# Kernel optimization log

Hardware: AMD Instinct MI355X
Metric: run time of the kernel (lower is better)

Reference implementation:

```python
import jax, jax.numpy as jnp
import numpy as np

EPS = 1e-5

def bn_eval(x, p):
    # p: [4, C] = gamma, beta, running_mean, running_var; channel-last broadcast
    g, b, m, v = p[0], p[1], p[2], p[3]
    return (x - m) * (g / jnp.sqrt(v + EPS)) + b

def _bn_params(k, c):
    k1, k2, k3, k4 = jax.random.split(k, 4)
    gamma = jax.random.uniform(k1, (c,)) + 0.5
    beta = jax.random.normal(k2, (c,)) * 0.1
    mean = jax.random.normal(k3, (c,)) * 0.1
    var = jax.random.uniform(k4, (c,)) + 0.5
    return jnp.stack([gamma, beta, mean, var])

def _lin(k, fan_in, fan_out):
    bound = 1.0 / np.sqrt(fan_in)
    kw, kb = jax.random.split(k)
    w = jax.random.uniform(kw, (fan_in, fan_out), minval=-bound, maxval=bound)
    b = jax.random.uniform(kb, (fan_out,), minval=-bound, maxval=bound)
    return w, b

def setup_inputs() -> dict:
    key = jax.random.key(0)
    B, N, S, C, G = 2, 4096, 16, 256, 8
    ks = jax.random.split(key, 20)
    feats = jax.random.normal(ks[0], (B, N, C), dtype=jnp.float32)
    coords = jax.random.normal(ks[1], (B, N, 3), dtype=jnp.float32)
    index = jax.random.randint(ks[2], (B, N, S), 0, N, dtype=jnp.int32)
    wq, bq = _lin(ks[3], C, C); bnq = _bn_params(ks[4], C)
    wk, bk = _lin(ks[5], C, C); bnk = _bn_params(ks[6], C)
    wv, bv = _lin(ks[7], C, C)
    pm_w1, pm_b1 = _lin(ks[8], 3, C); pm_bn = _bn_params(ks[9], C)
    pm_w2, pm_b2 = _lin(ks[10], C, C)
    pb_w1, pb_b1 = _lin(ks[11], 3, C); pb_bn = _bn_params(ks[12], C)
    pb_w2, pb_b2 = _lin(ks[13], C, C)
    we_w1, we_b1 = _lin(ks[14], C, G); we_bn = _bn_params(ks[15], G)
    we_w2, we_b2 = _lin(ks[16], G, G)
    return dict(feats=feats, coords=coords, index=index,
                wq=wq, bq=bq, bnq=bnq, wk=wk, bk=bk, bnk=bnk, wv=wv, bv=bv,
                pm_w1=pm_w1, pm_b1=pm_b1, pm_bn=pm_bn, pm_w2=pm_w2, pm_b2=pm_b2,
                pb_w1=pb_w1, pb_b1=pb_b1, pb_bn=pb_bn, pb_w2=pb_w2, pb_b2=pb_b2,
                we_w1=we_w1, we_b1=we_b1, we_bn=we_bn, we_w2=we_w2, we_b2=we_b2)

def reference(feats, coords, index,
              wq, bq, bnq, wk, bk, bnk, wv, bv,
              pm_w1, pm_b1, pm_bn, pm_w2, pm_b2,
              pb_w1, pb_b1, pb_bn, pb_w2, pb_b2,
              we_w1, we_b1, we_bn, we_w2, we_b2):
    B, N, C = feats.shape
    S = index.shape[2]
    G = we_w1.shape[1]
    q = jax.nn.relu(bn_eval(feats @ wq + bq, bnq))                       # [B,N,C]
    k = jax.nn.relu(bn_eval(feats @ wk + bk, bnk))                       # [B,N,C]
    v = feats @ wv + bv                                                   # [B,N,C]
    idx = index.reshape(B, N * S)
    key_g = jnp.take_along_axis(k, idx[:, :, None], axis=1).reshape(B, N, S, C)
    val_g = jnp.take_along_axis(v, idx[:, :, None], axis=1).reshape(B, N, S, C)
    crd_g = jnp.take_along_axis(coords, idx[:, :, None], axis=1).reshape(B, N, S, 3)
    relation_qk = key_g - q[:, :, None, :]                                # [B,N,S,C]
    pos = coords[:, :, None, :] - crd_g                                   # [B,N,S,3]
    pem = jax.nn.relu(bn_eval(pos @ pm_w1 + pm_b1, pm_bn)) @ pm_w2 + pm_b2
    relation_qk = relation_qk * pem
    peb = jax.nn.relu(bn_eval(pos @ pb_w1 + pb_b1, pb_bn)) @ pb_w2 + pb_b2
    relation_qk = relation_qk + peb
    val_g = val_g + peb
    w = jax.nn.relu(bn_eval(relation_qk @ we_w1 + we_b1, we_bn)) @ we_w2 + we_b2  # [B,N,S,G]
    w = jax.nn.softmax(w, axis=2)                                         # softmax over neighbors
    val_g = val_g.reshape(B, N, S, G, C // G)
    out = jnp.einsum('bnsgi,bnsg->bngi', val_g, w).reshape(B, N, C)
    return out
```

## Files before the change

kernel.cpp:

```cpp
#include <hip/hip_runtime.h>
#include <hip/hip_bf16.h>


typedef __attribute__((ext_vector_type(8))) short bf16x8_t;
typedef __attribute__((ext_vector_type(4))) float f32x4_t;

#define BN_EPS 1e-5f
#define WSYNC() asm volatile("s_waitcnt lgkmcnt(0)" ::: "memory")

__device__ __forceinline__ float blo(unsigned int v) {
    union { unsigned int u; float f; } x; x.u = v << 16; return x.f;
}
__device__ __forceinline__ float bhi(unsigned int v) {
    union { unsigned int u; float f; } x; x.u = v & 0xffff0000u; return x.f;
}
__device__ __forceinline__ unsigned int fbits(float f) {
    union { float f; unsigned int u; } x; x.f = f; return x.u;
}
__device__ __forceinline__ unsigned short f2b(float f) {
    unsigned int u = fbits(f);
    return (unsigned short)((u + 0x7fffu + ((u >> 16) & 1u)) >> 16);
}
__device__ __forceinline__ float b2f(unsigned short h) {
    union { unsigned int u; float f; } x; x.u = ((unsigned int)h) << 16; return x.f;
}
__device__ __forceinline__ unsigned int f2bpk(float a, float b) {
    union { __hip_bfloat162 h; unsigned int u; } x;
    x.h = __float22bfloat162_rn(make_float2(a, b));
    return x.u;
}
__device__ __forceinline__ unsigned int relpair(unsigned int kb, unsigned int qb,
                                                unsigned int pm_, unsigned int pb_) {
    float r0 = (blo(kb) - blo(qb)) * blo(pm_) + blo(pb_);
    float r1 = (bhi(kb) - bhi(qb)) * bhi(pm_) + bhi(pb_);
    return f2bpk(r0, r1);
}

__global__ __launch_bounds__(256) void k_prep(
    const float* __restrict__ wq, const float* __restrict__ wk,
    const float* __restrict__ wv, const float* __restrict__ pm2,
    const float* __restrict__ pb2,
    const float* __restrict__ pm_w1, const float* __restrict__ pm_b1,
    const float* __restrict__ pm_bn,
    const float* __restrict__ pb_w1, const float* __restrict__ pb_b1,
    const float* __restrict__ pb_bn,
    const float* __restrict__ we_w1,
    unsigned short* __restrict__ wsT, unsigned short* __restrict__ w1F,
    unsigned short* __restrict__ we1TF)
{
    const int bid = blockIdx.x, t = threadIdx.x;
    if (bid < 160) {
        __shared__ unsigned short T[32][72];
        const int mat = bid >> 5;
        const int kk  = (bid >> 2) & 7;
        const int ntq = bid & 3;
        const float* s = (mat == 0) ? wq : (mat == 1) ? wk : (mat == 2) ? wv
                         : (mat == 3) ? pm2 : pb2;
        {
            int c = t & 63, r0 = t >> 6;
            for (int i = 0; i < 8; ++i) {
                int r = r0 + i * 4;
                T[r][c] = f2b(s[(kk * 32 + r) * 256 + ntq * 64 + c]);
            }
        }
        __syncthreads();
        {
            int seg = t >> 6, lane = t & 63;
            int col = seg * 16 + (lane & 15);
            int kr  = (lane >> 4) * 8;
            unsigned int v[8];
            #pragma unroll
            for (int j = 0; j < 8; ++j) v[j] = T[kr + j][col];
            uint4 o;
            o.x = v[0] | (v[1] << 16);
            o.y = v[2] | (v[3] << 16);
            o.z = v[4] | (v[5] << 16);
            o.w = v[6] | (v[7] << 16);
            *(uint4*)(wsT + mat * 65536 + (ntq * 4 + seg) * 4096 + kk * 512 + lane * 8) = o;
        }
    } else if (bid == 160) {
        int c = t;
        int nt = c >> 4, l15 = c & 15;
        float sm = pm_bn[c] / sqrtf(pm_bn[768 + c] + BN_EPS);
        float sb = pb_bn[c] / sqrtf(pb_bn[768 + c] + BN_EPS);
        float W[2][4];
        W[0][0] = pm_w1[c] * sm; W[0][1] = pm_w1[256 + c] * sm;
        W[0][2] = pm_w1[512 + c] * sm;
        W[0][3] = (pm_b1[c] - pm_bn[512 + c]) * sm + pm_bn[256 + c];
        W[1][0] = pb_w1[c] * sb; W[1][1] = pb_w1[256 + c] * sb;
        W[1][2] = pb_w1[512 + c] * sb;
        W[1][3] = (pb_b1[c] - pb_bn[512 + c]) * sb + pb_bn[256 + c];
        for (int pass = 0; pass < 2; ++pass) {
            unsigned short xh = f2b(W[pass][0]), xl = f2b(W[pass][0] - b2f(xh));
            unsigned short yh = f2b(W[pass][1]), yl = f2b(W[pass][1] - b2f(yh));
            unsigned short zh = f2b(W[pass][2]), zl = f2b(W[pass][2] - b2f(zh));
            unsigned short bh = f2b(W[pass][3]), bl = f2b(W[pass][3] - b2f(bh));
            unsigned short sl[16] = { xh, xh, xl, yh, yh, yl, zh, zh, zl,
                                      bh, bl, 0, 0, 0, 0, 0 };
            for (int q = 0; q < 4; ++q)
                for (int j = 0; j < 8; ++j)
                    w1F[((pass * 16 + nt) * 64 + q * 16 + l15) * 8 + j] =
                        (q < 2) ? sl[q * 8 + j] : (unsigned short)0;
        }
    } else {
        for (int j = 0; j < 8; ++j) {
            int e = t * 8 + j;
            int g = e >> 8, c = e & 255;
            we1TF[g * 256 + c] = f2b(we_w1[c * 8 + g]);
        }
    }
}

__global__ __launch_bounds__(256) void k_qkv(
    const float* __restrict__ feats,
    const unsigned short* __restrict__ wT,
    const float* __restrict__ bq, const float* __restrict__ bnq,
    const float* __restrict__ bk, const float* __restrict__ bnk,
    const float* __restrict__ bv,
    unsigned short* __restrict__ qkv)
{
    __shared__ unsigned short A[32][264];
    const int t    = threadIdx.x;
    const int widx = blockIdx.x >> 8;
    const int mb   = blockIdx.x & 255;

    for (int i = 0; i < 8; ++i) {
        int row = 4 * i + (t >> 6), col = (t & 63) * 4;
        float4 f = *(const float4*)(feats + (mb * 32 + row) * 256 + col);
        *(uint2*)&A[row][col] = make_uint2(f2bpk(f.x, f.y), f2bpk(f.z, f.w));
    }
    __syncthreads();

    const int lane = t & 63, w = t >> 6;
    const int ln15 = lane & 15, quad = lane >> 4;
    const int mt = w & 1, nh = w >> 1;

    bf16x8_t afr[8];
    #pragma unroll
    for (int kk = 0; kk < 8; ++kk)
        afr[kk] = *(const bf16x8_t*)&A[mt * 16 + ln15][kk * 32 + quad * 8];

    const unsigned short* W = wT + widx * 65536;
    const float* bias = (widx == 0) ? bq : (widx == 1) ? bk : bv;
    const float* bn   = (widx == 0) ? bnq : (widx == 1) ? bnk : nullptr;
    unsigned short* dst = qkv + (size_t)widx * 8192 * 256;

    f32x4_t acc[8];
    for (int j = 0; j < 8; ++j) acc[j] = (f32x4_t){0.f, 0.f, 0.f, 0.f};

    #pragma unroll
    for (int kk = 0; kk < 8; ++kk) {
        #pragma unroll
        for (int j = 0; j < 8; ++j) {
            int nt = nh * 8 + j;
            bf16x8_t bfr = *(const bf16x8_t*)(W + ((nt * 8 + kk) * 64 + lane) * 8);
            acc[j] = __builtin_amdgcn_mfma_f32_16x16x32_bf16(afr[kk], bfr, acc[j], 0, 0, 0);
        }
    }

    float bb[8], sc[8], mu[8], be[8];
    #pragma unroll
    for (int j = 0; j < 8; ++j) {
        int c = (nh * 8 + j) * 16 + ln15;
        bb[j] = bias[c];
        if (bn) {
            sc[j] = bn[c] / sqrtf(bn[768 + c] + BN_EPS);
            be[j] = bn[256 + c];
            mu[j] = bn[512 + c];
        }
    }
    __syncthreads();
    #pragma unroll
    for (int j = 0; j < 8; ++j) {
        int c = (nh * 8 + j) * 16 + ln15;
        float y[4];
        for (int r = 0; r < 4; ++r) {
            y[r] = acc[j][r] + bb[j];
            if (bn) y[r] = fmaxf((y[r] - mu[j]) * sc[j] + be[j], 0.f);
        }
        for (int r = 0; r < 4; r += 2) {
            unsigned int pk = f2bpk(y[r], y[r + 1]);
            A[mt * 16 + quad * 4 + r][c]     = (unsigned short)pk;
            A[mt * 16 + quad * 4 + r + 1][c] = (unsigned short)(pk >> 16);
        }
    }
    __syncthreads();
    {
        int row = t >> 3, cc = (t & 7) * 32;
        #pragma unroll
        for (int j = 0; j < 4; ++j) {
            uint4 v = *(const uint4*)&A[row][cc + 8 * j];
            *(uint4*)(dst + (mb * 32 + row) * 256 + cc + 8 * j) = v;
        }
    }
}

__global__ __launch_bounds__(512, 4) void k_main(
    const float* __restrict__ coords,
    const int*   __restrict__ index,
    const unsigned short* __restrict__ qm,
    const unsigned short* __restrict__ km,
    const unsigned short* __restrict__ vm,
    const unsigned short* __restrict__ pmw2F,
    const unsigned short* __restrict__ pbw2F,
    const unsigned short* __restrict__ w1F,
    const unsigned short* __restrict__ we1TF,
    const float* __restrict__ pm_b2, const float* __restrict__ pb_b2,
    const float* __restrict__ we_b1, const float* __restrict__ we_bn,
    const float* __restrict__ we_w2, const float* __restrict__ we_b2,
    float* __restrict__ out)
{
    __shared__ unsigned short bufR[64][264];
    __shared__ unsigned short bufP[64][264];
    __shared__ unsigned short posX[64][32];
    __shared__ float usP[2][64][8];
    __shared__ float us_[64][8];
    __shared__ int   rowg_[64];
    __shared__ float we2s[8][8];
    __shared__ float web2[8], swe8[8], dwe8[8];

    const int t   = threadIdx.x;
    const int P0  = blockIdx.x * 4;
    const int bb_ = P0 >> 12;
    const int w = t >> 6, lane = t & 63;
    const int ln15 = lane & 15, quad = lane >> 4;
    const int p   = w >> 1, sub = w & 1;
    const int R0  = p * 16;
    const int Pg  = P0 + p;

    const int rg = (bb_ << 12) + index[Pg * 16 + ln15];
    uint4 kpre[4];
    #pragma unroll
    for (int kk = 0; kk < 4; ++kk)
        kpre[kk] = *(const uint4*)(km + rg * 256 + (sub * 4 + kk) * 32 + quad * 8);

    if (t < 64) {
        int m  = t;
        int Pr = P0 + (m >> 4);
        int rs = (bb_ << 12) + index[Pr * 16 + (m & 15)];
        rowg_[m] = rs;
        float x = coords[Pr * 3 + 0] - coords[rs * 3 + 0];
        float y = coords[Pr * 3 + 1] - coords[rs * 3 + 1];
        float z = coords[Pr * 3 + 2] - coords[rs * 3 + 2];
        unsigned short xh = f2b(x), xl = f2b(x - b2f(xh));
        unsigned short yh = f2b(y), yl = f2b(y - b2f(yh));
        unsigned short zh = f2b(z), zl = f2b(z - b2f(zh));
        const unsigned short one = 0x3f80;
        posX[m][0] = xh; posX[m][1] = xl; posX[m][2] = xh;
        posX[m][3] = yh; posX[m][4] = yl; posX[m][5] = yh;
        posX[m][6] = zh; posX[m][7] = zl; posX[m][8] = zh;
        posX[m][9] = one; posX[m][10] = one;
        #pragma unroll
        for (int j2 = 11; j2 < 32; ++j2) posX[m][j2] = 0;
        we2s[m >> 3][m & 7] = we_w2[m];
    }
    if (t < 8) {
        float s = we_bn[t] / sqrtf(we_bn[24 + t] + BN_EPS);
        swe8[t] = s;
        dwe8[t] = (we_b1[t] - we_bn[16 + t]) * s + we_bn[8 + t];
        web2[t] = we_b2[t];
    }
    __syncthreads();

    bf16x8_t afrP[4];
    #pragma unroll
    for (int mt = 0; mt < 4; ++mt)
        afrP[mt] = *(const bf16x8_t*)&posX[mt * 16 + ln15][quad * 8];

    {
        f32x4_t hb[2][4];
        for (int ntl = 0; ntl < 2; ++ntl)
            for (int mt = 0; mt < 4; ++mt) hb[ntl][mt] = (f32x4_t){0.f, 0.f, 0.f, 0.f};
        #pragma unroll
        for (int ntl = 0; ntl < 2; ++ntl) {
            int nt = w * 2 + ntl;
            bf16x8_t wfr = *(const bf16x8_t*)(w1F + ((16 + nt) * 64 + lane) * 8);
            #pragma unroll
            for (int mt = 0; mt < 4; ++mt)
                hb[ntl][mt] = __builtin_amdgcn_mfma_f32_16x16x32_bf16(wfr, afrP[mt], hb[ntl][mt], 0, 0, 0);
        }
        #pragma unroll
        for (int ntl = 0; ntl < 2; ++ntl) {
            int cb = w * 32 + ntl * 16 + quad * 4;
            #pragma unroll
            for (int mt = 0; mt < 4; ++mt) {
                unsigned int pk0 = f2bpk(fmaxf(hb[ntl][mt][0], 0.f), fmaxf(hb[ntl][mt][1], 0.f));
                unsigned int pk1 = f2bpk(fmaxf(hb[ntl][mt][2], 0.f), fmaxf(hb[ntl][mt][3], 0.f));
                *(uint2*)&bufR[mt * 16 + ln15][cb] = make_uint2(pk0, pk1);
            }
        }
    }
    __syncthreads();

    f32x4_t accM[2][4];
    for (int ntl = 0; ntl < 2; ++ntl)
        for (int mt = 0; mt < 4; ++mt) accM[ntl][mt] = (f32x4_t){0.f, 0.f, 0.f, 0.f};
    #pragma unroll
    for (int ntl = 0; ntl < 2; ++ntl) {
        int nt = w * 2 + ntl;
        bf16x8_t wfr = *(const bf16x8_t*)(w1F + (nt * 64 + lane) * 8);
        #pragma unroll
        for (int mt = 0; mt < 4; ++mt)
            accM[ntl][mt] = __builtin_amdgcn_mfma_f32_16x16x32_bf16(wfr, afrP[mt], accM[ntl][mt], 0, 0, 0);
    }
    f32x4_t acc[2][4];
    {
        f32x4_t b0 = *(const f32x4_t*)(pb_b2 + (w * 2    ) * 16 + quad * 4);
        f32x4_t b1 = *(const f32x4_t*)(pb_b2 + (w * 2 + 1) * 16 + quad * 4);
        for (int mt = 0; mt < 4; ++mt) { acc[0][mt] = b0; acc[1][mt] = b1; }
    }
    #pragma unroll
    for (int kk = 0; kk < 8; ++kk) {
        bf16x8_t afr[4];
        #pragma unroll
        for (int mt = 0; mt < 4; ++mt)
            afr[mt] = *(const bf16x8_t*)&bufR[mt * 16 + ln15][kk * 32 + quad * 8];
        #pragma unroll
        for (int ntl = 0; ntl < 2; ++ntl) {
            int nt = w * 2 + ntl;
            bf16x8_t wfr = *(const bf16x8_t*)(pbw2F + ((nt * 8 + kk) * 64 + lane) * 8);
            #pragma unroll
            for (int mt = 0; mt < 4; ++mt)
                acc[ntl][mt] = __builtin_amdgcn_mfma_f32_16x16x32_bf16(wfr, afr[mt], acc[ntl][mt], 0, 0, 0);
        }
    }
    #pragma unroll
    for (int ntl = 0; ntl < 2; ++ntl) {
        int cb = w * 32 + ntl * 16 + quad * 4;
        #pragma unroll
        for (int mt = 0; mt < 4; ++mt) {
            unsigned int pk0 = f2bpk(acc[ntl][mt][0], acc[ntl][mt][1]);
            unsigned int pk1 = f2bpk(acc[ntl][mt][2], acc[ntl][mt][3]);
            *(uint2*)&bufP[mt * 16 + ln15][cb] = make_uint2(pk0, pk1);
        }
    }
    __syncthreads();

    #pragma unroll
    for (int ntl = 0; ntl < 2; ++ntl) {
        int cb = w * 32 + ntl * 16 + quad * 4;
        #pragma unroll
        for (int mt = 0; mt < 4; ++mt) {
            unsigned int pk0 = f2bpk(fmaxf(accM[ntl][mt][0], 0.f), fmaxf(accM[ntl][mt][1], 0.f));
            unsigned int pk1 = f2bpk(fmaxf(accM[ntl][mt][2], 0.f), fmaxf(accM[ntl][mt][3], 0.f));
            *(uint2*)&bufR[mt * 16 + ln15][cb] = make_uint2(pk0, pk1);
        }
    }
    __syncthreads();

    uint4 qpre[4];
    #pragma unroll
    for (int kk = 0; kk < 4; ++kk)
        qpre[kk] = *(const uint4*)(qm + Pg * 256 + (sub * 4 + kk) * 32 + quad * 8);
    {
        f32x4_t b0 = *(const f32x4_t*)(pm_b2 + (w * 2    ) * 16 + quad * 4);
        f32x4_t b1 = *(const f32x4_t*)(pm_b2 + (w * 2 + 1) * 16 + quad * 4);
        for (int mt = 0; mt < 4; ++mt) { acc[0][mt] = b0; acc[1][mt] = b1; }
    }
    #pragma unroll
    for (int kk = 0; kk < 8; ++kk) {
        bf16x8_t afr[4];
        #pragma unroll
        for (int mt = 0; mt < 4; ++mt)
            afr[mt] = *(const bf16x8_t*)&bufR[mt * 16 + ln15][kk * 32 + quad * 8];
        #pragma unroll
        for (int ntl = 0; ntl < 2; ++ntl) {
            int nt = w * 2 + ntl;
            bf16x8_t wfr = *(const bf16x8_t*)(pmw2F + ((nt * 8 + kk) * 64 + lane) * 8);
            #pragma unroll
            for (int mt = 0; mt < 4; ++mt)
                acc[ntl][mt] = __builtin_amdgcn_mfma_f32_16x16x32_bf16(wfr, afr[mt], acc[ntl][mt], 0, 0, 0);
        }
    }
    __syncthreads();

    #pragma unroll
    for (int ntl = 0; ntl < 2; ++ntl) {
        int cb = w * 32 + ntl * 16 + quad * 4;
        #pragma unroll
        for (int mt = 0; mt < 4; ++mt) {
            unsigned int pk0 = f2bpk(acc[ntl][mt][0], acc[ntl][mt][1]);
            unsigned int pk1 = f2bpk(acc[ntl][mt][2], acc[ntl][mt][3]);
            *(uint2*)&bufR[mt * 16 + ln15][cb] = make_uint2(pk0, pk1);
        }
    }
    __syncthreads();

    {
        const bf16x8_t bz = {0, 0, 0, 0, 0, 0, 0, 0};
        f32x4_t lacc = {0.f, 0.f, 0.f, 0.f};
        #pragma unroll
        for (int kk = 0; kk < 4; ++kk) {
            int cb8 = (sub * 4 + kk) * 32 + quad * 8;
            uint4 pm4 = *(const uint4*)&bufR[R0 + ln15][cb8];
            uint4 pb4 = *(const uint4*)&bufP[R0 + ln15][cb8];
            uint4 q4  = qpre[kk];
            union { uint4 u; bf16x8_t v; } rr;
            rr.u.x = relpair(kpre[kk].x, q4.x, pm4.x, pb4.x);
            rr.u.y = relpair(kpre[kk].y, q4.y, pm4.y, pb4.y);
            rr.u.z = relpair(kpre[kk].z, q4.z, pm4.z, pb4.z);
            rr.u.w = relpair(kpre[kk].w, q4.w, pm4.w, pb4.w);
            bf16x8_t wfr = bz;
            if (ln15 < 8) wfr = *(const bf16x8_t*)(we1TF + ln15 * 256 + cb8);
            lacc = __builtin_amdgcn_mfma_f32_16x16x32_bf16(wfr, rr.v, lacc, 0, 0, 0);
        }
        if (quad < 2)
            *(f32x4_t*)&usP[sub][R0 + ln15][quad * 4] = lacc;
    }
    __syncthreads();

    if (sub == 0 && lane < 16) {
        int s = lane;
        float uv[8], l[8];
        #pragma unroll
        for (int g = 0; g < 8; ++g) {
            float x = usP[0][R0 + s][g] + usP[1][R0 + s][g];
            uv[g] = fmaxf(x * swe8[g] + dwe8[g], 0.f);
        }
        #pragma unroll
        for (int g = 0; g < 8; ++g) {
            float x = web2[g];
            for (int gp = 0; gp < 8; ++gp) x += uv[gp] * we2s[gp][g];
            l[g] = x;
        }
        #pragma unroll
        for (int g = 0; g < 8; ++g) us_[R0 + s][g] = l[g];
    }
    WSYNC();

    if (sub == 0 && lane < 8) {
        int g = lane;
        float mx = -1e30f;
        for (int s = 0; s < 16; ++s) mx = fmaxf(mx, us_[R0 + s][g]);
        float e[16], sum = 0.f;
        for (int s = 0; s < 16; ++s) { e[s] = __expf(us_[R0 + s][g] - mx); sum += e[s]; }
        float inv = 1.f / sum;
        for (int s = 0; s < 16; ++s) us_[R0 + s][g] = e[s] * inv;
    }
    __syncthreads();

    {
        int idx2 = sub * 64 + lane;
        int c5 = idx2 * 2, g = c5 >> 5;
        float a0 = 0.f, a1 = 0.f;
        #pragma unroll
        for (int s = 0; s < 16; ++s) {
            int rv = rowg_[R0 + s];
            float wv_ = us_[R0 + s][g];
            unsigned int v2 = *(const unsigned int*)(vm + rv * 256 + c5);
            unsigned int p2 = *(const unsigned int*)&bufP[R0 + s][c5];
            a0 += wv_ * (blo(v2) + blo(p2));
            a1 += wv_ * (bhi(v2) + bhi(p2));
        }
        *(float2*)(out + (size_t)Pg * 256 + c5) = make_float2(a0, a1);
    }
}

extern "C" void kernel_launch(void* const* d_in, const int* in_sizes, int n_in,
                              void* d_out, int out_size, void* d_ws, size_t ws_size,
                              hipStream_t stream)
{
    const float* feats  = (const float*)d_in[0];
    const float* coords = (const float*)d_in[1];
    const int*   index  = (const int*)d_in[2];
    const float* wq     = (const float*)d_in[3];
    const float* bq     = (const float*)d_in[4];
    const float* bnq    = (const float*)d_in[5];
    const float* wk     = (const float*)d_in[6];
    const float* bk     = (const float*)d_in[7];
    const float* bnk    = (const float*)d_in[8];
    const float* wv     = (const float*)d_in[9];
    const float* bv     = (const float*)d_in[10];
    const float* pm_w1  = (const float*)d_in[11];
    const float* pm_b1  = (const float*)d_in[12];
    const float* pm_bn  = (const float*)d_in[13];
    const float* pm_w2  = (const float*)d_in[14];
    const float* pm_b2  = (const float*)d_in[15];
    const float* pb_w1  = (const float*)d_in[16];
    const float* pb_b1  = (const float*)d_in[17];
    const float* pb_bn  = (const float*)d_in[18];
    const float* pb_w2  = (const float*)d_in[19];
    const float* pb_b2  = (const float*)d_in[20];
    const float* we_w1  = (const float*)d_in[21];
    const float* we_b1  = (const float*)d_in[22];
    const float* we_bn  = (const float*)d_in[23];
    const float* we_w2  = (const float*)d_in[24];
    const float* we_b2  = (const float*)d_in[25];

    unsigned short* qkv   = (unsigned short*)d_ws;
    unsigned short* wsT   = qkv + (size_t)3 * 8192 * 256;
    unsigned short* we1TF = wsT + 5 * 65536;
    unsigned short* w1F   = we1TF + 2048;

    const size_t need = (size_t)13275136;
    if (ws_size < need) {
        hipMemsetAsync(d_out, 0, (size_t)out_size * 4, stream);
        return;
    }

    k_prep<<<162,  256, 0, stream>>>(wq, wk, wv, pm_w2, pb_w2,
                                     pm_w1, pm_b1, pm_bn,
                                     pb_w1, pb_b1, pb_bn,
                                     we_w1, wsT, w1F, we1TF);
    k_qkv <<<768,  256, 0, stream>>>(feats, wsT, bq, bnq, bk, bnk, bv, qkv);
    k_main<<<2048, 512, 0, stream>>>(coords, index,
                                     qkv,
                                     qkv + (size_t)8192 * 256,
                                     qkv + (size_t)2 * 8192 * 256,
                                     wsT + 3 * 65536,
                                     wsT + 4 * 65536,
                                     w1F, we1TF,
                                     pm_b2, pb_b2,
                                     we_b1, we_bn, we_w2, we_b2,
                                     (float*)d_out);
}
```

Measured before the change: 191.3 us.

## Fold BN into scale/shift, drop LDS staging, split relation reduction per wave

Precomputes per-channel BN scale/shift for q/k/v in the prep kernel. k_qkv swaps the MFMA operand order so each lane writes four consecutive channels straight to global, removing the LDS staging and two barriers. In k_main each wave now covers the full 256-channel reduction for its own point, so the cross-subwave partial sums and block-level syncs go away. Value gathers are prefetched into registers using shuffled row indices. The cost is higher register pressure from 8 k/q prefetches plus 16 value loads per lane, which may hurt occupancy.

```diff
diff --git a/kernel.cpp b/kernel.cpp
--- a/kernel.cpp
+++ b/kernel.cpp
@@ -45,8 +45,11 @@
     const float* __restrict__ pb_w1, const float* __restrict__ pb_b1,
     const float* __restrict__ pb_bn,
     const float* __restrict__ we_w1,
+    const float* __restrict__ bq, const float* __restrict__ bnq,
+    const float* __restrict__ bk, const float* __restrict__ bnk,
+    const float* __restrict__ bv,
     unsigned short* __restrict__ wsT, unsigned short* __restrict__ w1F,
-    unsigned short* __restrict__ we1TF)
+    unsigned short* __restrict__ we1TF, float* __restrict__ SS)
 {
     const int bid = blockIdx.x, t = threadIdx.x;
     if (bid < 160) {
@@ -108,15 +111,22 @@
             int g = e >> 8, c = e & 255;
             we1TF[g * 256 + c] = f2b(we_w1[c * 8 + g]);
         }
+        int c = t;
+        float sq = bnq[c] / sqrtf(bnq[768 + c] + BN_EPS);
+        SS[c]        = sq;
+        SS[256 + c]  = (bq[c] - bnq[512 + c]) * sq + bnq[256 + c];
+        float sk = bnk[c] / sqrtf(bnk[768 + c] + BN_EPS);
+        SS[512 + c]  = sk;
+        SS[768 + c]  = (bk[c] - bnk[512 + c]) * sk + bnk[256 + c];
+        SS[1024 + c] = 1.0f;
+        SS[1280 + c] = bv[c];
     }
 }
 
 __global__ __launch_bounds__(256) void k_qkv(
     const float* __restrict__ feats,
     const unsigned short* __restrict__ wT,
-    const float* __restrict__ bq, const float* __restrict__ bnq,
-    const float* __restrict__ bk, const float* __restrict__ bnk,
-    const float* __restrict__ bv,
+    const float* __restrict__ SS,
     unsigned short* __restrict__ qkv)
 {
     __shared__ unsigned short A[32][264];
@@ -141,8 +151,6 @@
         afr[kk] = *(const bf16x8_t*)&A[mt * 16 + ln15][kk * 32 + quad * 8];
 
     const unsigned short* W = wT + widx * 65536;
-    const float* bias = (widx == 0) ? bq : (widx == 1) ? bk : bv;
-    const float* bn   = (widx == 0) ? bnq : (widx == 1) ? bnk : nullptr;
     unsigned short* dst = qkv + (size_t)widx * 8192 * 256;
 
     f32x4_t acc[8];
@@ -153,45 +161,28 @@
         #pragma unroll
         for (int j = 0; j < 8; ++j) {
             int nt = nh * 8 + j;
-            bf16x8_t bfr = *(const bf16x8_t*)(W + ((nt * 8 + kk) * 64 + lane) * 8);
-            acc[j] = __builtin_amdgcn_mfma_f32_16x16x32_bf16(afr[kk], bfr, acc[j], 0, 0, 0);
-        }
-    }
-
-    float bb[8], sc[8], mu[8], be[8];
+            bf16x8_t wfr = *(const bf16x8_t*)(W + ((nt * 8 + kk) * 64 + lane) * 8);
+            acc[j] = __builtin_amdgcn_mfma_f32_16x16x32_bf16(wfr, afr[kk], acc[j], 0, 0, 0);
+        }
+    }
+
+    const float* S = SS + widx * 512;
+    const int row = mb * 32 + mt * 16 + ln15;
     #pragma unroll
     for (int j = 0; j < 8; ++j) {
-        int c = (nh * 8 + j) * 16 + ln15;
-        bb[j] = bias[c];
-        if (bn) {
-            sc[j] = bn[c] / sqrtf(bn[768 + c] + BN_EPS);
-            be[j] = bn[256 + c];
-            mu[j] = bn[512 + c];
-        }
-    }
-    __syncthreads();
-    #pragma unroll
-    for (int j = 0; j < 8; ++j) {
-        int c = (nh * 8 + j) * 16 + ln15;
-        float y[4];
-        for (int r = 0; r < 4; ++r) {
-            y[r] = acc[j][r] + bb[j];
-            if (bn) y[r] = fmaxf((y[r] - mu[j]) * sc[j] + be[j], 0.f);
-        }
-        for (int r = 0; r < 4; r += 2) {
-            unsigned int pk = f2bpk(y[r], y[r + 1]);
-            A[mt * 16 + quad * 4 + r][c]     = (unsigned short)pk;
-            A[mt * 16 + quad * 4 + r + 1][c] = (unsigned short)(pk >> 16);
-        }
-    }
-    __syncthreads();
-    {
-        int row = t >> 3, cc = (t & 7) * 32;
-        #pragma unroll
-        for (int j = 0; j < 4; ++j) {
-            uint4 v = *(const uint4*)&A[row][cc + 8 * j];
-            *(uint4*)(dst + (mb * 32 + row) * 256 + cc + 8 * j) = v;
-        }
+        int n0 = (nh * 8 + j) * 16 + quad * 4;
+        float4 s4 = *(const float4*)(S + n0);
+        float4 h4 = *(const float4*)(S + 256 + n0);
+        float y0 = acc[j][0] * s4.x + h4.x;
+        float y1 = acc[j][1] * s4.y + h4.y;
+        float y2 = acc[j][2] * s4.z + h4.z;
+        float y3 = acc[j][3] * s4.w + h4.w;
+        if (widx < 2) {
+            y0 = fmaxf(y0, 0.f); y1 = fmaxf(y1, 0.f);
+            y2 = fmaxf(y2, 0.f); y3 = fmaxf(y3, 0.f);
+        }
+        *(uint2*)(dst + (size_t)row * 256 + n0) =
+            make_uint2(f2bpk(y0, y1), f2bpk(y2, y3));
     }
 }
 
@@ -213,9 +204,7 @@
     __shared__ unsigned short bufR[64][264];
     __shared__ unsigned short bufP[64][264];
     __shared__ unsigned short posX[64][32];
-    __shared__ float usP[2][64][8];
-    __shared__ float us_[64][8];
-    __shared__ int   rowg_[64];
+    __shared__ float us_[8][16][10];
     __shared__ float we2s[8][8];
     __shared__ float web2[8], swe8[8], dwe8[8];
 
@@ -229,16 +218,11 @@
     const int Pg  = P0 + p;
 
     const int rg = (bb_ << 12) + index[Pg * 16 + ln15];
-    uint4 kpre[4];
-    #pragma unroll
-    for (int kk = 0; kk < 4; ++kk)
-        kpre[kk] = *(const uint4*)(km + rg * 256 + (sub * 4 + kk) * 32 + quad * 8);
 
     if (t < 64) {
         int m  = t;
         int Pr = P0 + (m >> 4);
         int rs = (bb_ << 12) + index[Pr * 16 + (m & 15)];
-        rowg_[m] = rs;
         float x = coords[Pr * 3 + 0] - coords[rs * 3 + 0];
         float y = coords[Pr * 3 + 1] - coords[rs * 3 + 1];
         float z = coords[Pr * 3 + 2] - coords[rs * 3 + 2];
@@ -348,10 +332,10 @@
     }
     __syncthreads();
 
-    uint4 qpre[4];
-    #pragma unroll
-    for (int kk = 0; kk < 4; ++kk)
-        qpre[kk] = *(const uint4*)(qm + Pg * 256 + (sub * 4 + kk) * 32 + quad * 8);
+    uint4 kpre[8];
+    #pragma unroll
+    for (int kk = 0; kk < 8; ++kk)
+        kpre[kk] = *(const uint4*)(km + (size_t)rg * 256 + kk * 32 + quad * 8);
     {
         f32x4_t b0 = *(const f32x4_t*)(pm_b2 + (w * 2    ) * 16 + quad * 4);
         f32x4_t b1 = *(const f32x4_t*)(pm_b2 + (w * 2 + 1) * 16 + quad * 4);
@@ -374,6 +358,18 @@
     }
     __syncthreads();
 
+    uint4 qpre[8];
+    #pragma unroll
+    for (int kk = 0; kk < 8; ++kk)
+        qpre[kk] = *(const uint4*)(qm + (size_t)Pg * 256 + kk * 32 + quad * 8);
+    const int c5 = (sub * 64 + lane) * 2;
+    unsigned int vpre[16];
+    #pragma unroll
+    for (int s = 0; s < 16; ++s) {
+        int rv = __shfl(rg, s);
+        vpre[s] = *(const unsigned int*)(vm + (size_t)rv * 256 + c5);
+    }
+
     #pragma unroll
     for (int ntl = 0; ntl < 2; ++ntl) {
         int cb = w * 32 + ntl * 16 + quad * 4;
@@ -390,8 +386,8 @@
         const bf16x8_t bz = {0, 0, 0, 0, 0, 0, 0, 0};
         f32x4_t lacc = {0.f, 0.f, 0.f, 0.f};
         #pragma unroll
-        for (int kk = 0; kk < 4; ++kk) {
-            int cb8 = (sub * 4 + kk) * 32 + quad * 8;
+        for (int kk = 0; kk < 8; ++kk) {
+            int cb8 = kk * 32 + quad * 8;
             uint4 pm4 = *(const uint4*)&bufR[R0 + ln15][cb8];
             uint4 pb4 = *(const uint4*)&bufP[R0 + ln15][cb8];
             uint4 q4  = qpre[kk];
@@ -404,50 +400,52 @@
             if (ln15 < 8) wfr = *(const bf16x8_t*)(we1TF + ln15 * 256 + cb8);
             lacc = __builtin_amdgcn_mfma_f32_16x16x32_bf16(wfr, rr.v, lacc, 0, 0, 0);
         }
-        if (quad < 2)
-            *(f32x4_t*)&usP[sub][R0 + ln15][quad * 4] = lacc;
-    }
-    __syncthreads();
-
-    if (sub == 0 && lane < 16) {
+        if (quad < 2) {
+            f32x4_t uv4;
+            #pragma unroll
+            for (int r = 0; r < 4; ++r) {
+                int g = quad * 4 + r;
+                uv4[r] = fmaxf(lacc[r] * swe8[g] + dwe8[g], 0.f);
+            }
+            *(f32x4_t*)&us_[w][ln15][quad * 4] = uv4;
+        }
+    }
+    WSYNC();
+
+    if (lane < 16) {
         int s = lane;
-        float uv[8], l[8];
-        #pragma unroll
-        for (int g = 0; g < 8; ++g) {
-            float x = usP[0][R0 + s][g] + usP[1][R0 + s][g];
-            uv[g] = fmaxf(x * swe8[g] + dwe8[g], 0.f);
-        }
+        float uvv[8], l[8];
+        #pragma unroll
+        for (int g = 0; g < 8; ++g) uvv[g] = us_[w][s][g];
         #pragma unroll
         for (int g = 0; g < 8; ++g) {
             float x = web2[g];
-            for (int gp = 0; gp < 8; ++gp) x += uv[gp] * we2s[gp][g];
+            for (int gp = 0; gp < 8; ++gp) x += uvv[gp] * we2s[gp][g];
             l[g] = x;
         }
         #pragma unroll
-        for (int g = 0; g < 8; ++g) us_[R0 + s][g] = l[g];
+        for (int g = 0; g < 8; ++g) us_[w][s][g] = l[g];
     }
     WSYNC();
 
-    if (sub == 0 && lane < 8) {
+    if (lane < 8) {
         int g = lane;
         float mx = -1e30f;
-        for (int s = 0; s < 16; ++s) mx = fmaxf(mx, us_[R0 + s][g]);
+        for (int s = 0; s < 16; ++s) mx = fmaxf(mx, us_[w][s][g]);
         float e[16], sum = 0.f;
-        for (int s = 0; s < 16; ++s) { e[s] = __expf(us_[R0 + s][g] - mx); sum += e[s]; }
+        for (int s = 0; s < 16; ++s) { e[s] = __expf(us_[w][s][g] - mx); sum += e[s]; }
         float inv = 1.f / sum;
-        for (int s = 0; s < 16; ++s) us_[R0 + s][g] = e[s] * inv;
-    }
-    __syncthreads();
+        for (int s = 0; s < 16; ++s) us_[w][s][g] = e[s] * inv;
+    }
+    WSYNC();
 
     {
-        int idx2 = sub * 64 + lane;
-        int c5 = idx2 * 2, g = c5 >> 5;
+        int g = c5 >> 5;
         float a0 = 0.f, a1 = 0.f;
         #pragma unroll
         for (int s = 0; s < 16; ++s) {
-            int rv = rowg_[R0 + s];
-            float wv_ = us_[R0 + s][g];
-            unsigned int v2 = *(const unsigned int*)(vm + rv * 256 + c5);
+            float wv_ = us_[w][s][g];
+            unsigned int v2 = vpre[s];
             unsigned int p2 = *(const unsigned int*)&bufP[R0 + s][c5];
             a0 += wv_ * (blo(v2) + blo(p2));
             a1 += wv_ * (bhi(v2) + bhi(p2));
@@ -491,8 +489,9 @@
     unsigned short* wsT   = qkv + (size_t)3 * 8192 * 256;
     unsigned short* we1TF = wsT + 5 * 65536;
     unsigned short* w1F   = we1TF + 2048;
-
-    const size_t need = (size_t)13275136;
+    float*          SS    = (float*)(w1F + 16384);
+
+    const size_t need = (size_t)13281280;
     if (ws_size < need) {
         hipMemsetAsync(d_out, 0, (size_t)out_size * 4, stream);
         return;
@@ -501,8 +500,10 @@
     k_prep<<<162,  256, 0, stream>>>(wq, wk, wv, pm_w2, pb_w2,
                                      pm_w1, pm_b1, pm_bn,
                                      pb_w1, pb_b1, pb_bn,
-                                     we_w1, wsT, w1F, we1TF);
-    k_qkv <<<768,  256, 0, stream>>>(feats, wsT, bq, bnq, bk, bnk, bv, qkv);
+                                     we_w1,
+                                     bq, bnq, bk, bnk, bv,
+                                     wsT, w1F, we1TF, SS);
+    k_qkv <<<768,  256, 0, stream>>>(feats, wsT, SS, qkv);
     k_main<<<2048, 512, 0, stream>>>(coords, index,
                                      qkv,
                                      qkv + (size_t)8192 * 256,
```

Measured after the change: 212.4 us. 11.0% more time.
